# Kernel tuning notes

Measured on AMD Instinct MI355X. Metric: run time of the kernel, lower is better.

The kernel has to match this reference:

```python
import jax, jax.numpy as jnp
import numpy as np

N = 10000          # nodes
E = 160000         # edges (avg degree 16)
H = 32             # hidden_dim
ND = 64            # node_dim
ED = 16            # edge_dim
MH = 128           # edge_mlp_hidden
MP_STEPS = 3


def setup_inputs() -> dict:
    key = jax.random.key(0)
    ks = jax.random.split(key, 10)
    s = lambda d: 1.0 / np.sqrt(d)
    return {
        "x": jax.random.normal(ks[0], (N, ND), jnp.float32),
        "edge_index": jax.random.randint(ks[1], (2, E), 0, N, dtype=jnp.int64),
        "edge_attr": jax.random.normal(ks[2], (E, ED), jnp.float32),
        # node_proj: Linear(node_dim -> hidden_dim)
        "Wp": jax.random.normal(ks[3], (ND, H), jnp.float32) * s(ND),
        "bp": jnp.zeros((H,), jnp.float32),
        # edge network MLP: edge_dim -> MH -> H*H
        "W1": jax.random.normal(ks[4], (ED, MH), jnp.float32) * s(ED),
        "b1": jnp.zeros((MH,), jnp.float32),
        "W2": jax.random.normal(ks[5], (MH, H * H), jnp.float32) * s(MH),
        "b2": jnp.zeros((H * H,), jnp.float32),
        # GRUCell params (torch layout: stacked [r, z, n], shape (3H, H))
        "w_ih": jax.random.normal(ks[6], (3 * H, H), jnp.float32) * s(H),
        "w_hh": jax.random.normal(ks[7], (3 * H, H), jnp.float32) * s(H),
        "b_ih": jnp.zeros((3 * H,), jnp.float32),
        "b_hh": jnp.zeros((3 * H,), jnp.float32),
    }


def gru_cell(x, h, w_ih, w_hh, b_ih, b_hh):
    # torch.nn.GRUCell semantics, gates stacked [r, z, n]
    gi = x @ w_ih.T + b_ih
    gh = h @ w_hh.T + b_hh
    i_r, i_z, i_n = jnp.split(gi, 3, axis=-1)
    h_r, h_z, h_n = jnp.split(gh, 3, axis=-1)
    r = jax.nn.sigmoid(i_r + h_r)
    z = jax.nn.sigmoid(i_z + h_z)
    n = jnp.tanh(i_n + r * h_n)
    return (1.0 - z) * n + z * h


def reference(x, edge_index, edge_attr, Wp, bp, W1, b1, W2, b2, w_ih, w_hh, b_ih, b_hh):
    h = x @ Wp + bp  # (N, H)
    # per-edge weight matrices; edge_attr is loop-invariant so compute once
    We = (jax.nn.relu(edge_attr @ W1 + b1) @ W2 + b2).reshape(E, H, H)
    src = edge_index[0]  # h_j (message source)
    dst = edge_index[1]  # aggregation target (PyG source_to_target flow)
    for _ in range(MP_STEPS):
        msg = jnp.einsum('eij,ej->ei', We, h[src])          # (E, H) per-edge GEMV
        agg = jax.ops.segment_sum(msg, dst, num_segments=N)  # scatter-add
        h = gru_cell(agg, h, w_ih, w_hh, b_ih, b_hh)
    return h
```

## Files before the change

### kernel.cpp

```cpp
#include <hip/hip_runtime.h>
#include <stdint.h>

#define H   32
#define ND  64
#define ED  16
#define MH  128
#define HH  1024

__device__ __forceinline__ float bf2f(uint16_t u) {
    union { uint32_t u; float f; } v; v.u = ((uint32_t)u) << 16; return v.f;
}
__device__ __forceinline__ uint16_t f2bf(float f) {
    union { float f; uint32_t u; } v; v.f = f;
    return (uint16_t)((v.u + 0x7FFFu + ((v.u >> 16) & 1u)) >> 16);
}
__device__ __forceinline__ float ldf(const void* p, size_t i, int isf32) {
    return isf32 ? ((const float*)p)[i] : bf2f(((const uint16_t*)p)[i]);
}

__global__ void k_detect(const uint16_t* __restrict__ xr,
                         const int* __restrict__ ei, int nedges,
                         int* __restrict__ flags) {
    __shared__ int s_bad, s_hi;
    int t = threadIdx.x;
    if (t == 0) { s_bad = 0; s_hi = 0; }
    __syncthreads();
    int bad = 0;
    for (int i = t; i < 2048; i += 256) {
        uint16_t u = xr[i];
        int e = (u >> 7) & 0xFF;
        if (!(u == 0 || (e >= 96 && e <= 144))) bad++;
    }
    atomicAdd(&s_bad, bad);
    int mm = nedges < 4096 ? nedges : 4096;
    int hi = 0;
    for (int i = t; i < mm; i += 256) hi |= (ei[2 * i + 1] != 0);
    if (hi) atomicOr(&s_hi, 1);
    __syncthreads();
    if (t == 0) {
        flags[0] = (s_bad > 204) ? 1 : 0;
        flags[1] = (s_hi == 0) ? 1 : 0;
    }
}

__device__ __forceinline__ int load_idx(const int* __restrict__ ei, int is64,
                                        long long pos, int nnodes) {
    int v = is64 ? (int)(((const long long*)ei)[pos]) : ei[pos];
    v = v < 0 ? 0 : v;
    return v >= nnodes ? nnodes - 1 : v;
}

__global__ void k_hist(const int* __restrict__ ei, const int* __restrict__ flags,
                       int* __restrict__ deg, int nedges, int nnodes) {
    int e = blockIdx.x * 256 + threadIdx.x;
    if (e >= nedges) return;
    int s = load_idx(ei, flags[1], e, nnodes);
    atomicAdd(&deg[s], 1);
}

__global__ void k_scan(const int* __restrict__ deg, int* __restrict__ cursor,
                       int nnodes) {
    __shared__ int tot[256];
    int t = threadIdx.x;
    int C = (nnodes + 255) >> 8;
    int b = t * C, e = b + C < nnodes ? b + C : nnodes;
    int s = 0;
    for (int i = b; i < e; i++) s += deg[i];
    tot[t] = s;
    __syncthreads();
    if (t == 0) {
        int acc = 0;
        for (int i = 0; i < 256; i++) { int v = tot[i]; tot[i] = acc; acc += v; }
    }
    __syncthreads();
    int acc = tot[t];
    for (int i = b; i < e; i++) { cursor[i] = acc; acc += deg[i]; }
}

__global__ void k_scatter(const int* __restrict__ ei, const int* __restrict__ flags,
                          int* __restrict__ cursor, int* __restrict__ perm,
                          int nedges, int nnodes) {
    int e = blockIdx.x * 256 + threadIdx.x;
    if (e >= nedges) return;
    int s = load_idx(ei, flags[1], e, nnodes);
    int p = atomicAdd(&cursor[s], 1);
    perm[p] = e;
}

__global__ __launch_bounds__(256) void k_node_proj(
    const void* __restrict__ x, const void* __restrict__ wp,
    const void* __restrict__ bp, float* __restrict__ h, int nnodes,
    const int* __restrict__ flags)
{
    __shared__ float wp_s[ND][H];
    __shared__ float x_s[8][ND + 1];
    int isf32 = flags[0];
    int t = threadIdx.x;
    for (int i = t; i < ND * H; i += 256) wp_s[i >> 5][i & 31] = ldf(wp, i, isf32);
    for (int i = t; i < 8 * ND; i += 256) {
        int row = i >> 6, col = i & 63;
        int gn = blockIdx.x * 8 + row;
        x_s[row][col] = (gn < nnodes) ? ldf(x, (size_t)gn * ND + col, isf32) : 0.f;
    }
    __syncthreads();
    int nl = t >> 5, c = t & 31;
    int n = blockIdx.x * 8 + nl;
    if (n >= nnodes) return;
    float acc = ldf(bp, c, isf32);
#pragma unroll
    for (int k = 0; k < ND; k++) acc += x_s[nl][k] * wp_s[k][c];
    h[(size_t)n * H + c] = acc;
}

__global__ void k_permw2(const void* __restrict__ w2g, float* __restrict__ Bp,
                         const int* __restrict__ flags) {
    int isf32 = flags[0];
    int idx = blockIdx.x * 256 + threadIdx.x;
    if (idx >= MH * HH) return;
    int k = idx / HH, col = idx % HH;
    int i = col >> 5, j = col & 31;
    Bp[(size_t)j * 4096 + i * 128 + k] = ldf(w2g, idx, isf32);
}

__global__ __launch_bounds__(256) void k_T6(
    const float* __restrict__ Bp, const float* __restrict__ h,
    float* __restrict__ Tall, int nnodes)
{
    __shared__ float h_s[128 * 33];
    __shared__ float occ_pad[12288];
    int t = threadIdx.x;
    int cbq = blockIdx.x & 7;
    int n0 = (blockIdx.x >> 3) * 128;
    int c = cbq * 512 + t * 2;

    if (nnodes < 0) occ_pad[t] = h[t];

    for (int i = t; i < 128 * 32; i += 256) {
        int n = i >> 5, j = i & 31;
        h_s[n * 33 + j] = (n0 + n < nnodes) ? h[(size_t)(n0 + n) * H + j] : 0.f;
    }
    float2 Breg[32];
#pragma unroll
    for (int j = 0; j < 32; j++)
        Breg[j] = *((const float2*)&Bp[(size_t)j * 4096 + c]);
    __syncthreads();

    int nmax = nnodes - n0; if (nmax > 128) nmax = 128;
    int n = 0;
    for (; n + 2 <= nmax; n += 2) {
        float2 a0 = {0.f, 0.f}, a1 = {0.f, 0.f};
#pragma unroll
        for (int j = 0; j < 32; j++) {
            float h0 = h_s[n * 33 + j], h1 = h_s[(n + 1) * 33 + j];
            float2 b = Breg[j];
            a0.x += h0 * b.x; a0.y += h0 * b.y;
            a1.x += h1 * b.x; a1.y += h1 * b.y;
        }
        *((float2*)&Tall[(size_t)(n0 + n) * 4096 + c]) = a0;
        *((float2*)&Tall[(size_t)(n0 + n + 1) * 4096 + c]) = a1;
    }
    if (n < nmax) {
        float2 a0 = {0.f, 0.f};
#pragma unroll
        for (int j = 0; j < 32; j++) {
            float h0 = h_s[n * 33 + j];
            float2 b = Breg[j];
            a0.x += h0 * b.x; a0.y += h0 * b.y;
        }
        *((float2*)&Tall[(size_t)(n0 + n) * 4096 + c]) = a0;
    }
}

__global__ __launch_bounds__(256) void k_u(
    const void* __restrict__ b2g, const float* __restrict__ h,
    float* __restrict__ u, int nnodes, const int* __restrict__ flags)
{
    __shared__ float b2_s[32 * 33];
    __shared__ float h_s[8 * 32];
    int isf32 = flags[0];
    int t = threadIdx.x;
    int n0 = blockIdx.x * 8;
    for (int idx = t; idx < 1024; idx += 256) {
        int i = idx >> 5, j = idx & 31;
        b2_s[i * 33 + j] = ldf(b2g, idx, isf32);
    }
    for (int i = t; i < 8 * 32; i += 256) {
        int n = i >> 5;
        h_s[i] = (n0 + n < nnodes) ? h[(size_t)(n0 + n) * H + (i & 31)] : 0.f;
    }
    __syncthreads();
    int nl = t >> 5, i = t & 31;
    if (n0 + nl >= nnodes) return;
    float acc = 0.f;
#pragma unroll
    for (int j = 0; j < 32; j++) acc += b2_s[i * 33 + j] * h_s[nl * 32 + j];
    u[(size_t)(n0 + nl) * 32 + i] = acc;
}

__global__ __launch_bounds__(256) void k_edge4(
    const void* __restrict__ ea, const void* __restrict__ w1,
    const void* __restrict__ b1g, const float* __restrict__ Tall,
    const float* __restrict__ u, const int* __restrict__ ei,
    const int* __restrict__ perm, const int* __restrict__ degp,
    const int* __restrict__ rendp, const int* __restrict__ flags,
    float* __restrict__ agg, int nedges, int nnodes)
{
    int n = blockIdx.x;
    int dcount = degp[n];
    if (dcount == 0) return;
    int rstart = rendp[n] - dcount;

    __shared__ float T_lds[32 * 132];
    __shared__ float hid_s[16 * 132];
    __shared__ float w1_s[ED * MH];
    __shared__ float ea_f[16 * ED];
    __shared__ float b1_s[MH];
    __shared__ float u_lds[32];
    __shared__ int   e_s[16], d_s[16];

    int t = threadIdx.x;
    int isf32 = flags[0], is64 = flags[1];

    for (int f = t; f < 1024; f += 256) {
        float4 q = *((const float4*)&Tall[(size_t)n * 4096 + f * 4]);
        int i = f >> 5, k4 = (f & 31) * 4;
        *((float4*)&T_lds[i * 132 + k4]) = q;
    }
    for (int i = t; i < ED * MH; i += 256) w1_s[i] = ldf(w1, i, isf32);
    if (t < MH) b1_s[t] = ldf(b1g, t, isf32);
    if (t < 32) u_lds[t] = u[(size_t)n * 32 + t];

    int e_rel = t & 15, i2 = t >> 4;
    int nchunks = (dcount + 15) >> 4;

    for (int ch = 0; ch < nchunks; ch++) {
        __syncthreads();
        if (t < 16) {
            int idx = ch * 16 + t;
            int e = (idx < dcount) ? perm[rstart + idx] : -1;
            e_s[t] = e;
            d_s[t] = (e >= 0) ? load_idx(ei, is64, (long long)nedges + e, nnodes) : 0;
        }
        __syncthreads();
        for (int i = t; i < 16 * ED; i += 256) {
            int e = e_s[i >> 4];
            ea_f[i] = (e >= 0) ? ldf(ea, (size_t)e * ED + (i & 15), isf32) : 0.f;
        }
        __syncthreads();
        for (int idx = t; idx < 16 * MH; idx += 256) {
            int el = idx >> 7, c = idx & 127;
            float acc = b1_s[c];
#pragma unroll
            for (int k = 0; k < ED; k++)
                acc += ea_f[el * ED + k] * w1_s[k * MH + c];
            hid_s[el * 132 + c] = fmaxf(acc, 0.f);
        }
        __syncthreads();
        if (e_s[e_rel] >= 0) {
            float a0 = u_lds[i2], a1 = u_lds[i2 + 16];
#pragma unroll
            for (int k4 = 0; k4 < 32; k4++) {
                float4 hv = *((const float4*)&hid_s[e_rel * 132 + k4 * 4]);
                float4 t0 = *((const float4*)&T_lds[i2 * 132 + k4 * 4]);
                float4 t1 = *((const float4*)&T_lds[(i2 + 16) * 132 + k4 * 4]);
                a0 += hv.x * t0.x + hv.y * t0.y + hv.z * t0.z + hv.w * t0.w;
                a1 += hv.x * t1.x + hv.y * t1.y + hv.z * t1.z + hv.w * t1.w;
            }
            int d = d_s[e_rel];
            atomicAdd(&agg[(size_t)d * H + i2], a0);
            atomicAdd(&agg[(size_t)d * H + i2 + 16], a1);
        }
    }
}

__global__ __launch_bounds__(256) void k_msg_valu(
    const void* __restrict__ ea, const void* __restrict__ w1,
    const void* __restrict__ b1g, const void* __restrict__ w2g,
    const void* __restrict__ b2g, const float* __restrict__ h,
    const int* __restrict__ ei, const int* __restrict__ flags,
    float* __restrict__ agg, int nedges, int nnodes)
{
    __shared__ float hid_s[64 * 130];
    __shared__ float w1_s[ED * MH];
    __shared__ float b1_s[MH];
    __shared__ float ea_f[64 * ED];

    int t = threadIdx.x;
    int e0 = blockIdx.x * 64;
    int isf32 = flags[0], is64 = flags[1];

    for (int i = t; i < 64 * ED; i += 256) {
        int e = e0 + (i >> 4);
        ea_f[i] = (e < nedges) ? ldf(ea, (size_t)e * ED + (i & 15), isf32) : 0.f;
    }
    for (int i = t; i < ED * MH; i += 256) w1_s[i] = ldf(w1, i, isf32);
    for (int i = t; i < MH; i += 256) b1_s[i] = ldf(b1g, i, isf32);
    __syncthreads();

    for (int idx = t; idx < 64 * MH; idx += 256) {
        int el = idx >> 7, c = idx & 127;
        float acc = b1_s[c];
#pragma unroll
        for (int k = 0; k < ED; k++)
            acc += ea_f[el * ED + k] * w1_s[k * MH + c];
        hid_s[el * 130 + c] = fmaxf(acc, 0.f);
    }
    __syncthreads();

    int lane = t & 63, w = t >> 6;
    int b = w * 64 + lane;
    int j = b & 31;
    int q = b >> 5;

    float b2v[4];
#pragma unroll
    for (int m = 0; m < 4; m++) b2v[m] = ldf(b2g, b + 256 * m, isf32);

    for (int g = 0; g < 4; g++) {
        float acc[16][4];
#pragma unroll
        for (int e = 0; e < 16; e++)
#pragma unroll
            for (int m = 0; m < 4; m++) acc[e][m] = 0.f;

        for (int k2 = 0; k2 < 64; k2++) {
            float w2a[4], w2b[4];
#pragma unroll
            for (int m = 0; m < 4; m++) {
                w2a[m] = ldf(w2g, (size_t)(2 * k2) * HH + b + 256 * m, isf32);
                w2b[m] = ldf(w2g, (size_t)(2 * k2 + 1) * HH + b + 256 * m, isf32);
            }
#pragma unroll
            for (int e = 0; e < 16; e++) {
                float2 hv = *((const float2*)&hid_s[(g * 16 + e) * 130 + 2 * k2]);
#pragma unroll
                for (int m = 0; m < 4; m++)
                    acc[e][m] += hv.x * w2a[m] + hv.y * w2b[m];
            }
        }

#pragma unroll
        for (int e = 0; e < 16; e++) {
            int eg = e0 + g * 16 + e;
            int valid = (eg < nedges);
            int se = valid ? load_idx(ei, is64, eg, nnodes) : 0;
            float he = h[(size_t)se * H + j];
            int d = valid ? load_idx(ei, is64, (long long)nedges + eg, nnodes) : 0;
#pragma unroll
            for (int m = 0; m < 4; m++) {
                float p = (acc[e][m] + b2v[m]) * he;
                p += __shfl_xor(p, 1);
                p += __shfl_xor(p, 2);
                p += __shfl_xor(p, 4);
                p += __shfl_xor(p, 8);
                p += __shfl_xor(p, 16);
                if ((lane & 31) == 0 && valid)
                    atomicAdd(&agg[(size_t)d * H + (q + 8 * m)], p);
            }
        }
    }
}

__global__ __launch_bounds__(256) void k_gru(
    const float* __restrict__ agg, float* hin,
    const void* __restrict__ w_ih, const void* __restrict__ w_hh,
    const void* __restrict__ b_ih, const void* __restrict__ b_hh,
    float* __restrict__ hout, void* __restrict__ out_any,
    int nnodes, int finalstep, const int* __restrict__ flags)
{
    __shared__ float wih_s[3 * H][H + 1];
    __shared__ float whh_s[3 * H][H + 1];
    __shared__ float bih_s[3 * H], bhh_s[3 * H];
    __shared__ float a_s[8][H + 1], h_s[8][H + 1];
    int isf32 = flags[0];
    int t = threadIdx.x;
    for (int i = t; i < 3 * H * H; i += 256) {
        wih_s[i >> 5][i & 31] = ldf(w_ih, i, isf32);
        whh_s[i >> 5][i & 31] = ldf(w_hh, i, isf32);
    }
    for (int i = t; i < 3 * H; i += 256) {
        bih_s[i] = ldf(b_ih, i, isf32);
        bhh_s[i] = ldf(b_hh, i, isf32);
    }
    int nl = t >> 5, i = t & 31;
    int n = blockIdx.x * 8 + nl;
    if (n < nnodes) {
        a_s[nl][i] = agg[(size_t)n * H + i];
        h_s[nl][i] = hin[(size_t)n * H + i];
    }
    __syncthreads();
    if (n >= nnodes) return;

    float gr = bih_s[i], gz = bih_s[H + i], gn = bih_s[2 * H + i];
    float hr = bhh_s[i], hz = bhh_s[H + i], hn = bhh_s[2 * H + i];
#pragma unroll
    for (int jj = 0; jj < H; jj++) {
        float a = a_s[nl][jj], hh = h_s[nl][jj];
        gr += a * wih_s[i][jj];      gz += a * wih_s[H + i][jj];  gn += a * wih_s[2 * H + i][jj];
        hr += hh * whh_s[i][jj];     hz += hh * whh_s[H + i][jj]; hn += hh * whh_s[2 * H + i][jj];
    }
    float r  = 1.f / (1.f + __expf(-(gr + hr)));
    float z  = 1.f / (1.f + __expf(-(gz + hz)));
    float nv = tanhf(gn + r * hn);
    float hnew = (1.f - z) * nv + z * h_s[nl][i];
    hout[(size_t)n * H + i] = hnew;
    hin[(size_t)n * H + i] = 0.f;
    if (finalstep) {
        if (isf32) ((float*)out_any)[(size_t)n * H + i] = hnew;
        else       ((uint16_t*)out_any)[(size_t)n * H + i] = f2bf(hnew);
    }
}

extern "C" void kernel_launch(void* const* d_in, const int* in_sizes, int n_in,
                              void* d_out, int out_size, void* d_ws, size_t ws_size,
                              hipStream_t stream)
{
    const void* x   = d_in[0];
    const int*  ei  = (const int*)d_in[1];
    const void* ea  = d_in[2];
    const void* wp  = d_in[3];
    const void* bp  = d_in[4];
    const void* w1  = d_in[5];
    const void* b1  = d_in[6];
    const void* w2  = d_in[7];
    const void* b2  = d_in[8];
    const void* wih = d_in[9];
    const void* whh = d_in[10];
    const void* bih = d_in[11];
    const void* bhh = d_in[12];

    int nnodes = in_sizes[0] / ND;
    int nedges = in_sizes[1] / 2;

    size_t hbytes = (size_t)nnodes * H * sizeof(float);
    size_t tbytes = (size_t)nnodes * 4096 * sizeof(float);
    if (ws_size < 256 + 2 * hbytes) return;

    size_t off = 0;
    int*   flags  = (int*)d_ws;                 off += 256;
    float* bufA   = (float*)((char*)d_ws + off); off += hbytes;
    float* bufB   = (float*)((char*)d_ws + off); off += hbytes;
    float* u_buf  = (float*)((char*)d_ws + off); off += hbytes;
    int*   deg    = (int*)((char*)d_ws + off);   off += (size_t)nnodes * 4;
    int*   cursor = (int*)((char*)d_ws + off);   off += (size_t)nnodes * 4;
    int*   perm   = (int*)((char*)d_ws + off);   off += (size_t)nedges * 4;
    off = (off + 255) & ~(size_t)255;
    float* Bperm  = (float*)((char*)d_ws + off); off += (size_t)MH * HH * 4;
    off = (off + 255) & ~(size_t)255;
    float* Tall   = (float*)((char*)d_ws + off); off += tbytes;
    int hi_tier = (ws_size >= off);

    k_detect<<<1, 256, 0, stream>>>((const uint16_t*)x, ei, nedges, flags);
    k_node_proj<<<(nnodes + 7) / 8, 256, 0, stream>>>(x, wp, bp, bufA, nnodes, flags);
    hipMemsetAsync(bufB, 0, hbytes, stream);

    if (hi_tier) {
        hipMemsetAsync(deg, 0, (size_t)nnodes * 4, stream);
        k_hist<<<(nedges + 255) / 256, 256, 0, stream>>>(ei, flags, deg, nedges, nnodes);
        k_scan<<<1, 256, 0, stream>>>(deg, cursor, nnodes);
        k_scatter<<<(nedges + 255) / 256, 256, 0, stream>>>(ei, flags, cursor, perm, nedges, nnodes);
        k_permw2<<<(MH * HH + 255) / 256, 256, 0, stream>>>(w2, Bperm, flags);
    }

    float* hcur = bufA;
    float* aggb = bufB;
    for (int s = 0; s < 3; s++) {
        if (hi_tier) {
            k_T6<<<((nnodes + 127) / 128) * 8, 256, 0, stream>>>(
                Bperm, hcur, Tall, nnodes);
            k_u<<<(nnodes + 7) / 8, 256, 0, stream>>>(b2, hcur, u_buf, nnodes, flags);
            k_edge4<<<nnodes, 256, 0, stream>>>(
                ea, w1, b1, Tall, u_buf, ei, perm, deg, cursor, flags,
                aggb, nedges, nnodes);
        } else {
            k_msg_valu<<<(nedges + 63) / 64, 256, 0, stream>>>(
                ea, w1, b1, w2, b2, hcur, ei, flags, aggb, nedges, nnodes);
        }
        k_gru<<<(nnodes + 7) / 8, 256, 0, stream>>>(
            aggb, hcur, wih, whh, bih, bhh, aggb, d_out, nnodes, s == 2, flags);
        float* tmp = hcur; hcur = aggb; aggb = tmp;
    }
}
```

Measured before the change: 810.6 us.

## Fuse u computation into projection/GRU and process two source nodes per edge block

Removes the separate k_u kernel by computing u = b2-projection of h inside k_node_proj (step 0) and inside k_gru for the next step. The edge kernel now handles two consecutive source nodes per block, loading both T tiles into LDS and mixing their edges into shared 16-edge chunks, which halves block count and cuts partially filled chunks for low-degree nodes. This costs double the LDS for T (lower occupancy) and extra syncs in the GRU kernel.

```diff
diff --git a/kernel.cpp b/kernel.cpp
--- a/kernel.cpp
+++ b/kernel.cpp
@@ -89,11 +89,14 @@
 
 __global__ __launch_bounds__(256) void k_node_proj(
     const void* __restrict__ x, const void* __restrict__ wp,
-    const void* __restrict__ bp, float* __restrict__ h, int nnodes,
-    const int* __restrict__ flags)
+    const void* __restrict__ bp, const void* __restrict__ b2g,
+    float* __restrict__ h, float* __restrict__ u0, int nnodes,
+    int emit_u, const int* __restrict__ flags)
 {
     __shared__ float wp_s[ND][H];
     __shared__ float x_s[8][ND + 1];
+    __shared__ float hn_s[8][33];
+    __shared__ float b2_s[32 * 33];
     int isf32 = flags[0];
     int t = threadIdx.x;
     for (int i = t; i < ND * H; i += 256) wp_s[i >> 5][i & 31] = ldf(wp, i, isf32);
@@ -102,14 +105,29 @@
         int gn = blockIdx.x * 8 + row;
         x_s[row][col] = (gn < nnodes) ? ldf(x, (size_t)gn * ND + col, isf32) : 0.f;
     }
+    if (emit_u)
+        for (int i = t; i < 1024; i += 256)
+            b2_s[(i >> 5) * 33 + (i & 31)] = ldf(b2g, i, isf32);
     __syncthreads();
     int nl = t >> 5, c = t & 31;
     int n = blockIdx.x * 8 + nl;
-    if (n >= nnodes) return;
-    float acc = ldf(bp, c, isf32);
-#pragma unroll
-    for (int k = 0; k < ND; k++) acc += x_s[nl][k] * wp_s[k][c];
-    h[(size_t)n * H + c] = acc;
+    int act = (n < nnodes);
+    if (act) {
+        float acc = ldf(bp, c, isf32);
+#pragma unroll
+        for (int k = 0; k < ND; k++) acc += x_s[nl][k] * wp_s[k][c];
+        h[(size_t)n * H + c] = acc;
+        hn_s[nl][c] = acc;
+    }
+    if (emit_u) {
+        __syncthreads();
+        if (act) {
+            float au = 0.f;
+#pragma unroll
+            for (int j = 0; j < 32; j++) au += b2_s[c * 33 + j] * hn_s[nl][j];
+            u0[(size_t)n * 32 + c] = au;
+        }
+    }
 }
 
 __global__ void k_permw2(const void* __restrict__ w2g, float* __restrict__ Bp,
@@ -171,33 +189,7 @@
     }
 }
 
-__global__ __launch_bounds__(256) void k_u(
-    const void* __restrict__ b2g, const float* __restrict__ h,
-    float* __restrict__ u, int nnodes, const int* __restrict__ flags)
-{
-    __shared__ float b2_s[32 * 33];
-    __shared__ float h_s[8 * 32];
-    int isf32 = flags[0];
-    int t = threadIdx.x;
-    int n0 = blockIdx.x * 8;
-    for (int idx = t; idx < 1024; idx += 256) {
-        int i = idx >> 5, j = idx & 31;
-        b2_s[i * 33 + j] = ldf(b2g, idx, isf32);
-    }
-    for (int i = t; i < 8 * 32; i += 256) {
-        int n = i >> 5;
-        h_s[i] = (n0 + n < nnodes) ? h[(size_t)(n0 + n) * H + (i & 31)] : 0.f;
-    }
-    __syncthreads();
-    int nl = t >> 5, i = t & 31;
-    if (n0 + nl >= nnodes) return;
-    float acc = 0.f;
-#pragma unroll
-    for (int j = 0; j < 32; j++) acc += b2_s[i * 33 + j] * h_s[nl * 32 + j];
-    u[(size_t)(n0 + nl) * 32 + i] = acc;
-}
-
-__global__ __launch_bounds__(256) void k_edge4(
+__global__ __launch_bounds__(256) void k_edge6(
     const void* __restrict__ ea, const void* __restrict__ w1,
     const void* __restrict__ b1g, const float* __restrict__ Tall,
     const float* __restrict__ u, const int* __restrict__ ei,
@@ -205,40 +197,53 @@
     const int* __restrict__ rendp, const int* __restrict__ flags,
     float* __restrict__ agg, int nedges, int nnodes)
 {
-    int n = blockIdx.x;
-    int dcount = degp[n];
-    if (dcount == 0) return;
-    int rstart = rendp[n] - dcount;
-
-    __shared__ float T_lds[32 * 132];
+    int nA = blockIdx.x * 2;
+    int hasB = (nA + 1 < nnodes);
+    int endA = rendp[nA], degA = degp[nA];
+    int start = endA - degA;
+    int endB = hasB ? rendp[nA + 1] : endA;
+    int total = endB - start;
+    if (total == 0) return;
+
+    __shared__ float T_lds[2 * 4224];
     __shared__ float hid_s[16 * 132];
     __shared__ float w1_s[ED * MH];
     __shared__ float ea_f[16 * ED];
     __shared__ float b1_s[MH];
-    __shared__ float u_lds[32];
-    __shared__ int   e_s[16], d_s[16];
+    __shared__ float u_lds[64];
+    __shared__ int   e_s[16], d_s[16], src_s[16];
 
     int t = threadIdx.x;
     int isf32 = flags[0], is64 = flags[1];
 
-    for (int f = t; f < 1024; f += 256) {
-        float4 q = *((const float4*)&Tall[(size_t)n * 4096 + f * 4]);
-        int i = f >> 5, k4 = (f & 31) * 4;
-        *((float4*)&T_lds[i * 132 + k4]) = q;
+    for (int f = t; f < 2048; f += 256) {
+        int sel = f >> 10, fi = f & 1023;
+        int node = nA + sel;
+        if (node < nnodes) {
+            float4 q = *((const float4*)&Tall[(size_t)node * 4096 + fi * 4]);
+            int i = fi >> 5, k4 = (fi & 31) * 4;
+            *((float4*)&T_lds[sel * 4224 + i * 132 + k4]) = q;
+        }
     }
     for (int i = t; i < ED * MH; i += 256) w1_s[i] = ldf(w1, i, isf32);
     if (t < MH) b1_s[t] = ldf(b1g, t, isf32);
-    if (t < 32) u_lds[t] = u[(size_t)n * 32 + t];
+    if (t < 64) {
+        int node = nA + (t >> 5);
+        u_lds[t] = (node < nnodes) ? u[(size_t)node * 32 + (t & 31)] : 0.f;
+    }
 
     int e_rel = t & 15, i2 = t >> 4;
-    int nchunks = (dcount + 15) >> 4;
+    int nchunks = (total + 15) >> 4;
 
     for (int ch = 0; ch < nchunks; ch++) {
         __syncthreads();
         if (t < 16) {
             int idx = ch * 16 + t;
-            int e = (idx < dcount) ? perm[rstart + idx] : -1;
+            int p = start + idx;
+            int valid = (idx < total);
+            int e = valid ? perm[p] : -1;
             e_s[t] = e;
+            src_s[t] = (valid && p >= endA) ? 1 : 0;
             d_s[t] = (e >= 0) ? load_idx(ei, is64, (long long)nedges + e, nnodes) : 0;
         }
         __syncthreads();
@@ -257,12 +262,14 @@
         }
         __syncthreads();
         if (e_s[e_rel] >= 0) {
-            float a0 = u_lds[i2], a1 = u_lds[i2 + 16];
+            int sel = src_s[e_rel];
+            int tb = sel * 4224;
+            float a0 = u_lds[sel * 32 + i2], a1 = u_lds[sel * 32 + i2 + 16];
 #pragma unroll
             for (int k4 = 0; k4 < 32; k4++) {
                 float4 hv = *((const float4*)&hid_s[e_rel * 132 + k4 * 4]);
-                float4 t0 = *((const float4*)&T_lds[i2 * 132 + k4 * 4]);
-                float4 t1 = *((const float4*)&T_lds[(i2 + 16) * 132 + k4 * 4]);
+                float4 t0 = *((const float4*)&T_lds[tb + i2 * 132 + k4 * 4]);
+                float4 t1 = *((const float4*)&T_lds[tb + (i2 + 16) * 132 + k4 * 4]);
                 a0 += hv.x * t0.x + hv.y * t0.y + hv.z * t0.z + hv.w * t0.w;
                 a1 += hv.x * t1.x + hv.y * t1.y + hv.z * t1.z + hv.w * t1.w;
             }
@@ -365,13 +372,15 @@
     const float* __restrict__ agg, float* hin,
     const void* __restrict__ w_ih, const void* __restrict__ w_hh,
     const void* __restrict__ b_ih, const void* __restrict__ b_hh,
+    const void* __restrict__ b2g, float* __restrict__ u_next,
     float* __restrict__ hout, void* __restrict__ out_any,
-    int nnodes, int finalstep, const int* __restrict__ flags)
+    int nnodes, int finalstep, int emit_u, const int* __restrict__ flags)
 {
     __shared__ float wih_s[3 * H][H + 1];
     __shared__ float whh_s[3 * H][H + 1];
     __shared__ float bih_s[3 * H], bhh_s[3 * H];
-    __shared__ float a_s[8][H + 1], h_s[8][H + 1];
+    __shared__ float a_s[8][H + 1], h_s[8][H + 1], hn_s[8][33];
+    __shared__ float b2_s[32 * 33];
     int isf32 = flags[0];
     int t = threadIdx.x;
     for (int i = t; i < 3 * H * H; i += 256) {
@@ -382,32 +391,47 @@
         bih_s[i] = ldf(b_ih, i, isf32);
         bhh_s[i] = ldf(b_hh, i, isf32);
     }
+    if (emit_u && !finalstep)
+        for (int i = t; i < 1024; i += 256)
+            b2_s[(i >> 5) * 33 + (i & 31)] = ldf(b2g, i, isf32);
     int nl = t >> 5, i = t & 31;
     int n = blockIdx.x * 8 + nl;
-    if (n < nnodes) {
+    int act = (n < nnodes);
+    if (act) {
         a_s[nl][i] = agg[(size_t)n * H + i];
         h_s[nl][i] = hin[(size_t)n * H + i];
     }
     __syncthreads();
-    if (n >= nnodes) return;
-
-    float gr = bih_s[i], gz = bih_s[H + i], gn = bih_s[2 * H + i];
-    float hr = bhh_s[i], hz = bhh_s[H + i], hn = bhh_s[2 * H + i];
-#pragma unroll
-    for (int jj = 0; jj < H; jj++) {
-        float a = a_s[nl][jj], hh = h_s[nl][jj];
-        gr += a * wih_s[i][jj];      gz += a * wih_s[H + i][jj];  gn += a * wih_s[2 * H + i][jj];
-        hr += hh * whh_s[i][jj];     hz += hh * whh_s[H + i][jj]; hn += hh * whh_s[2 * H + i][jj];
-    }
-    float r  = 1.f / (1.f + __expf(-(gr + hr)));
-    float z  = 1.f / (1.f + __expf(-(gz + hz)));
-    float nv = tanhf(gn + r * hn);
-    float hnew = (1.f - z) * nv + z * h_s[nl][i];
-    hout[(size_t)n * H + i] = hnew;
-    hin[(size_t)n * H + i] = 0.f;
-    if (finalstep) {
-        if (isf32) ((float*)out_any)[(size_t)n * H + i] = hnew;
-        else       ((uint16_t*)out_any)[(size_t)n * H + i] = f2bf(hnew);
+
+    if (act) {
+        float gr = bih_s[i], gz = bih_s[H + i], gn = bih_s[2 * H + i];
+        float hr = bhh_s[i], hz = bhh_s[H + i], hn = bhh_s[2 * H + i];
+#pragma unroll
+        for (int jj = 0; jj < H; jj++) {
+            float a = a_s[nl][jj], hh = h_s[nl][jj];
+            gr += a * wih_s[i][jj];      gz += a * wih_s[H + i][jj];  gn += a * wih_s[2 * H + i][jj];
+            hr += hh * whh_s[i][jj];     hz += hh * whh_s[H + i][jj]; hn += hh * whh_s[2 * H + i][jj];
+        }
+        float r  = 1.f / (1.f + __expf(-(gr + hr)));
+        float z  = 1.f / (1.f + __expf(-(gz + hz)));
+        float nv = tanhf(gn + r * hn);
+        float hnew = (1.f - z) * nv + z * h_s[nl][i];
+        hout[(size_t)n * H + i] = hnew;
+        hin[(size_t)n * H + i] = 0.f;
+        hn_s[nl][i] = hnew;
+        if (finalstep) {
+            if (isf32) ((float*)out_any)[(size_t)n * H + i] = hnew;
+            else       ((uint16_t*)out_any)[(size_t)n * H + i] = f2bf(hnew);
+        }
+    }
+    if (emit_u && !finalstep) {
+        __syncthreads();
+        if (act) {
+            float au = 0.f;
+#pragma unroll
+            for (int j = 0; j < 32; j++) au += b2_s[i * 33 + j] * hn_s[nl][j];
+            u_next[(size_t)n * 32 + i] = au;
+        }
     }
 }
 
@@ -451,7 +475,8 @@
     int hi_tier = (ws_size >= off);
 
     k_detect<<<1, 256, 0, stream>>>((const uint16_t*)x, ei, nedges, flags);
-    k_node_proj<<<(nnodes + 7) / 8, 256, 0, stream>>>(x, wp, bp, bufA, nnodes, flags);
+    k_node_proj<<<(nnodes + 7) / 8, 256, 0, stream>>>(
+        x, wp, bp, b2, bufA, u_buf, nnodes, hi_tier, flags);
     hipMemsetAsync(bufB, 0, hbytes, stream);
 
     if (hi_tier) {
@@ -468,8 +493,7 @@
         if (hi_tier) {
             k_T6<<<((nnodes + 127) / 128) * 8, 256, 0, stream>>>(
                 Bperm, hcur, Tall, nnodes);
-            k_u<<<(nnodes + 7) / 8, 256, 0, stream>>>(b2, hcur, u_buf, nnodes, flags);
-            k_edge4<<<nnodes, 256, 0, stream>>>(
+            k_edge6<<<(nnodes + 1) / 2, 256, 0, stream>>>(
                 ea, w1, b1, Tall, u_buf, ei, perm, deg, cursor, flags,
                 aggb, nedges, nnodes);
         } else {
@@ -477,7 +501,8 @@
                 ea, w1, b1, w2, b2, hcur, ei, flags, aggb, nedges, nnodes);
         }
         k_gru<<<(nnodes + 7) / 8, 256, 0, stream>>>(
-            aggb, hcur, wih, whh, bih, bhh, aggb, d_out, nnodes, s == 2, flags);
+            aggb, hcur, wih, whh, bih, bhh, b2, u_buf, aggb, d_out,
+            nnodes, s == 2, hi_tier, flags);
         float* tmp = hcur; hcur = aggb; aggb = tmp;
     }
 }
```

Measured after the change: 840.5 us. +3.7%, slower.
